# Performance work log

Measured on AMD Instinct MI355X. Metric: run time of the kernel, lower is better.

The kernel has to match this reference:

```python
import jax, jax.numpy as jnp
import numpy as np

N, D, K = 65536, 128, 2048  # n_cells, latent_dim, nmb_prototypes


def setup_inputs() -> dict:
    key = jax.random.key(0)
    k1, k2, k3, k4, k5 = jax.random.split(key, 5)
    x = jax.random.normal(k1, (N, D), dtype=jnp.float32)
    # nn.Linear default init scale ~ 1/sqrt(fan_in)
    W_proto = jax.random.normal(k2, (K, D), dtype=jnp.float32) * (1.0 / np.sqrt(D))
    recon_loss = jax.random.uniform(k3, (), dtype=jnp.float32)
    kl_loss = jax.random.uniform(k4, (), dtype=jnp.float32)
    mmd_loss = jax.random.uniform(k5, (), dtype=jnp.float32)
    return {"x": x, "W_proto": W_proto, "recon_loss": recon_loss,
            "kl_loss": kl_loss, "mmd_loss": mmd_loss}


def _pairwise_dist(z, w):
    # torch.cdist(z, w, p=2) via the matmul expansion (use_mm_for_euclid_dist)
    zz = jnp.sum(z * z, axis=1, keepdims=True)       # [N, 1]
    ww = jnp.sum(w * w, axis=1, keepdims=True).T     # [1, K]
    sq = zz + ww - 2.0 * (z @ w.T)                   # [N, K]
    return jnp.sqrt(jnp.maximum(sq, 0.0))


def reference(x, W_proto, recon_loss, kl_loss, mmd_loss):
    # cvae loss combination (compute_cvae_loss, calc_alpha_coeff = 0.5)
    cvae_loss = recon_loss + 0.5 * kl_loss + mmd_loss
    # F.normalize(x, dim=1, p=2): x / max(||x||_2, eps)
    nrm = jnp.maximum(jnp.linalg.norm(x, axis=1, keepdims=True), 1e-12)
    z = x / nrm                                      # [N, D]
    # self.prototypes(x): Linear without bias
    logits = z @ W_proto.T                           # [N, K]
    # prototype_decoding_loss: one NxK distance matrix reduced two ways
    dist = _pairwise_dist(z, W_proto)                # [N, K]
    propagation = jnp.mean(jnp.min(dist, axis=1))    # nearest prototype per cell
    emb_similarity = jnp.mean(jnp.min(dist, axis=0))  # nearest cell per prototype
    # forward returns (x, x, prototypes(x), cvae_loss, (prop, emb_sim)); x duplicated
    return (z, logits, cvae_loss, propagation, emb_similarity)
```

## Files before the change

### kernel.cpp

```cpp
#include <hip/hip_runtime.h>
#include <hip/hip_bf16.h>
#include <math.h>

#define N_CELLS 65536
#define D_DIM   128
#define K_PROTO 2048

typedef __attribute__((ext_vector_type(8))) short bf16x8;
typedef __attribute__((ext_vector_type(4))) float f32x4;

__device__ __forceinline__ unsigned int map_f2u(float f) {
  unsigned int u = __float_as_uint(f);
  return (u & 0x80000000u) ? ~u : (u | 0x80000000u);
}
__device__ __forceinline__ float unmap_u2f(unsigned int u) {
  unsigned int b = (u & 0x80000000u) ? (u ^ 0x80000000u) : ~u;
  return __uint_as_float(b);
}

__device__ __forceinline__ unsigned int f2bf(float f) {
  unsigned int u = __float_as_uint(f);
  return ((u + 0x7FFFu + ((u >> 16) & 1u)) >> 16) & 0xFFFFu;
}

__global__ __launch_bounds__(256) void normalize_k(
    const float* __restrict__ x, float* __restrict__ z,
    unsigned int* __restrict__ zb, unsigned int* __restrict__ rowmin_u) {
  int tid = threadIdx.x;
  int sub = tid & 31;
  int row = blockIdx.x * 8 + (tid >> 5);
  const f32x4* xr = (const f32x4*)(x + (size_t)row * D_DIM);
  f32x4 v = xr[sub];
  float s = v.x * v.x + v.y * v.y + v.z * v.z + v.w * v.w;
  #pragma unroll
  for (int off = 1; off < 32; off <<= 1) s += __shfl_xor(s, off, 64);
  float inv = 1.0f / fmaxf(sqrtf(s), 1e-12f);
  f32x4 zv = v * inv;
  __builtin_nontemporal_store(zv, (f32x4*)(z + (size_t)row * D_DIM) + sub);
  unsigned int lo = (f2bf(zv.y) << 16) | f2bf(zv.x);
  unsigned int h2 = (f2bf(zv.w) << 16) | f2bf(zv.z);
  unsigned long long pk = ((unsigned long long)h2 << 32) | lo;
  *((unsigned long long*)(zb + (size_t)row * (D_DIM / 2)) + sub) = pk;
  if (sub == 0) rowmin_u[row] = 0xFFFFFFFFu;
}

__global__ __launch_bounds__(256) void wprep_k(
    const float* __restrict__ W, unsigned int* __restrict__ wb,
    float* __restrict__ ww, unsigned int* __restrict__ colmax_u,
    const float* __restrict__ recon, const float* __restrict__ kl,
    const float* __restrict__ mmd, float* __restrict__ scal) {
  if (blockIdx.x == 0 && threadIdx.x == 0) {
    scal[0] = recon[0] + 0.5f * kl[0] + mmd[0];
  }
  int tid = threadIdx.x;
  int sub = tid & 31;
  int row = blockIdx.x * 8 + (tid >> 5);
  const f32x4* wr = (const f32x4*)(W + (size_t)row * D_DIM);
  f32x4 v = wr[sub];
  float s = v.x * v.x + v.y * v.y + v.z * v.z + v.w * v.w;
  #pragma unroll
  for (int off = 1; off < 32; off <<= 1) s += __shfl_xor(s, off, 64);
  if (sub == 0) {
    ww[row] = s;
    colmax_u[row] = 0u;
  }
  unsigned int lo = (f2bf(v.y) << 16) | f2bf(v.x);
  unsigned int h2 = (f2bf(v.w) << 16) | f2bf(v.z);
  unsigned long long pk = ((unsigned long long)h2 << 32) | lo;
  *((unsigned long long*)(wb + (size_t)row * (D_DIM / 2)) + sub) = pk;
}

__global__ __launch_bounds__(256) void gemm_k(
    const unsigned short* __restrict__ zb, const unsigned short* __restrict__ wb,
    const float* __restrict__ ww, float* __restrict__ logits,
    unsigned int* __restrict__ rowmin_u, unsigned int* __restrict__ colmax_u) {
  __shared__ float cs[128 * 128];

  int bid = blockIdx.x;
  int swz = (bid & 7) * 1024 + (bid >> 3);
  int nt  = swz & 15;
  int mt  = swz >> 4;

  int tid  = threadIdx.x;
  int lane = tid & 63;
  int wid  = tid >> 6;
  int wrow = (wid >> 1) * 64;
  int wcol = (wid & 1) * 64;
  int l15  = lane & 15;
  int hi   = lane >> 4;

  const char* Abase = (const char*)zb + ((size_t)(mt * 128 + wrow + l15) * 256 + hi * 16);
  const char* Bbase = (const char*)wb + ((size_t)(nt * 128 + wcol + l15) * 256 + hi * 16);

  f32x4 acc[4][4];
  #pragma unroll
  for (int i = 0; i < 4; ++i)
    #pragma unroll
    for (int j = 0; j < 4; ++j)
      acc[i][j] = f32x4{0.f, 0.f, 0.f, 0.f};

  #pragma unroll
  for (int kk = 0; kk < 4; ++kk) {
    bf16x8 a[4], b[4];
    #pragma unroll
    for (int i = 0; i < 4; ++i) a[i] = *(const bf16x8*)(Abase + i * 4096 + kk * 64);
    #pragma unroll
    for (int j = 0; j < 4; ++j) b[j] = *(const bf16x8*)(Bbase + j * 4096 + kk * 64);
    #pragma unroll
    for (int i = 0; i < 4; ++i)
      #pragma unroll
      for (int j = 0; j < 4; ++j)
        acc[i][j] = __builtin_amdgcn_mfma_f32_16x16x32_bf16(b[j], a[i], acc[i][j], 0, 0, 0);
  }

  size_t growbase = (size_t)mt * 128 + wrow;
  int    gcolbase = nt * 128 + wcol;

  f32x4 wwj[4];
  #pragma unroll
  for (int j = 0; j < 4; ++j)
    wwj[j] = *(const f32x4*)(ww + gcolbase + j * 16 + hi * 4);

  #pragma unroll
  for (int i = 0; i < 4; ++i) {
    size_t row = growbase + (size_t)(i * 16 + l15);
    float vmin = 1e30f;
    #pragma unroll
    for (int j = 0; j < 4; ++j) {
      #pragma unroll
      for (int r = 0; r < 4; ++r) vmin = fminf(vmin, wwj[j][r] - 2.0f * acc[i][j][r]);
    }
    vmin = fminf(vmin, __shfl_xor(vmin, 16, 64));
    vmin = fminf(vmin, __shfl_xor(vmin, 32, 64));
    if (hi == 0) atomicMin(&rowmin_u[row], map_f2u(vmin));
  }

  #pragma unroll
  for (int j = 0; j < 4; ++j) {
    f32x4 m = acc[0][j];
    #pragma unroll
    for (int i = 1; i < 4; ++i)
      #pragma unroll
      for (int r = 0; r < 4; ++r) m[r] = fmaxf(m[r], acc[i][j][r]);
    #pragma unroll
    for (int s2 = 1; s2 < 16; s2 <<= 1)
      #pragma unroll
      for (int r = 0; r < 4; ++r) m[r] = fmaxf(m[r], __shfl_xor(m[r], s2, 64));
    if (l15 == 0) {
      #pragma unroll
      for (int r = 0; r < 4; ++r)
        atomicMax(&colmax_u[gcolbase + j * 16 + hi * 4 + r], map_f2u(m[r]));
    }
  }

  #pragma unroll
  for (int i = 0; i < 4; ++i) {
    int row = wrow + i * 16 + l15;
    #pragma unroll
    for (int j = 0; j < 4; ++j) {
      int g  = (wcol >> 2) + j * 4 + hi;
      int pg = g ^ ((row & 7) << 2);
      *(f32x4*)((char*)cs + row * 512 + pg * 16) = acc[i][j];
    }
  }
  __syncthreads();

  {
    int l31  = lane & 31;
    int rsub = lane >> 5;
    #pragma unroll
    for (int it = 0; it < 16; ++it) {
      int row = it * 8 + wid * 2 + rsub;
      int pg  = l31 ^ ((row & 7) << 2);
      f32x4 c = *(const f32x4*)((const char*)cs + row * 512 + pg * 16);
      size_t grow = (size_t)mt * 128 + row;
      __builtin_nontemporal_store(c, (f32x4*)(logits + grow * K_PROTO + nt * 128 + l31 * 4));
    }
  }
}

__global__ __launch_bounds__(1024) void prop_k(
    const unsigned int* __restrict__ rowmin_u, float* __restrict__ out) {
  __shared__ float sbuf[16];
  const uint4* p = (const uint4*)rowmin_u;
  float s = 0.f;
  #pragma unroll
  for (int k = 0; k < 16; ++k) {
    uint4 u = p[threadIdx.x + 1024 * k];
    s += sqrtf(fmaxf(1.0f + unmap_u2f(u.x), 0.0f));
    s += sqrtf(fmaxf(1.0f + unmap_u2f(u.y), 0.0f));
    s += sqrtf(fmaxf(1.0f + unmap_u2f(u.z), 0.0f));
    s += sqrtf(fmaxf(1.0f + unmap_u2f(u.w), 0.0f));
  }
  #pragma unroll
  for (int off = 1; off < 64; off <<= 1) s += __shfl_xor(s, off, 64);
  int wid = threadIdx.x >> 6, lane = threadIdx.x & 63;
  if (lane == 0) sbuf[wid] = s;
  __syncthreads();
  if (threadIdx.x == 0) {
    float t = 0.f;
    #pragma unroll
    for (int w = 0; w < 16; ++w) t += sbuf[w];
    out[0] = t * (1.0f / N_CELLS);
  }
}

__global__ __launch_bounds__(1024) void emb_k(
    const unsigned int* __restrict__ colmax_u, const float* __restrict__ ww,
    float* __restrict__ out) {
  __shared__ float sbuf[16];
  float s = 0.f;
  for (int idx = threadIdx.x; idx < K_PROTO; idx += 1024)
    s += sqrtf(fmaxf(1.0f + ww[idx] - 2.0f * unmap_u2f(colmax_u[idx]), 0.0f));
  #pragma unroll
  for (int off = 1; off < 64; off <<= 1) s += __shfl_xor(s, off, 64);
  int wid = threadIdx.x >> 6, lane = threadIdx.x & 63;
  if (lane == 0) sbuf[wid] = s;
  __syncthreads();
  if (threadIdx.x == 0) {
    float t = 0.f;
    #pragma unroll
    for (int w = 0; w < 16; ++w) t += sbuf[w];
    out[0] = t * (1.0f / K_PROTO);
  }
}

extern "C" void kernel_launch(void* const* d_in, const int* in_sizes, int n_in,
                              void* d_out, int out_size, void* d_ws, size_t ws_size,
                              hipStream_t stream) {
  const float* x     = (const float*)d_in[0];
  const float* W     = (const float*)d_in[1];
  const float* recon = (const float*)d_in[2];
  const float* kl    = (const float*)d_in[3];
  const float* mmd   = (const float*)d_in[4];

  float* out    = (float*)d_out;
  float* z      = out;
  float* logits = out + (size_t)N_CELLS * D_DIM;
  float* scal   = logits + (size_t)N_CELLS * K_PROTO;

  char* ws = (char*)d_ws;
  unsigned int* zb = (unsigned int*)ws;
  size_t off = (size_t)N_CELLS * D_DIM * 2;
  unsigned int* wb = (unsigned int*)(ws + off);
  off += (size_t)K_PROTO * D_DIM * 2;
  float* ww = (float*)(ws + off);
  off += (size_t)K_PROTO * 4;
  unsigned int* rowmin_u = (unsigned int*)(ws + off);
  off += (size_t)N_CELLS * 4;
  unsigned int* colmax_u = (unsigned int*)(ws + off);

  normalize_k<<<N_CELLS / 8, 256, 0, stream>>>(x, z, zb, rowmin_u);
  wprep_k<<<K_PROTO / 8, 256, 0, stream>>>(W, wb, ww, colmax_u, recon, kl, mmd, scal);
  gemm_k<<<(N_CELLS / 128) * (K_PROTO / 128), 256, 0, stream>>>(
      (const unsigned short*)zb, (const unsigned short*)wb, ww, logits,
      rowmin_u, colmax_u);
  prop_k<<<1, 1024, 0, stream>>>(rowmin_u, scal + 1);
  emb_k<<<1, 1024, 0, stream>>>(colmax_u, ww, scal + 2);
}
```

Measured before the change: 206.4 us.

## Replace global atomic min/max with per-tile partials and multi-block reductions

The GEMM epilogue no longer issues global atomicMin/atomicMax for row minima and column maxima. Each tile now combines its warp results in shared memory and writes one partial per row and column to workspace buffers. Separate multi-block kernels reduce those partials, and a small final kernel combines the block sums. This removes atomic contention and the init writes, at the cost of an extra launch and more workspace traffic (about 4MB each for row and column partials).

```diff
diff --git a/kernel.cpp b/kernel.cpp
--- a/kernel.cpp
+++ b/kernel.cpp
@@ -9,15 +9,6 @@
 typedef __attribute__((ext_vector_type(8))) short bf16x8;
 typedef __attribute__((ext_vector_type(4))) float f32x4;
 
-__device__ __forceinline__ unsigned int map_f2u(float f) {
-  unsigned int u = __float_as_uint(f);
-  return (u & 0x80000000u) ? ~u : (u | 0x80000000u);
-}
-__device__ __forceinline__ float unmap_u2f(unsigned int u) {
-  unsigned int b = (u & 0x80000000u) ? (u ^ 0x80000000u) : ~u;
-  return __uint_as_float(b);
-}
-
 __device__ __forceinline__ unsigned int f2bf(float f) {
   unsigned int u = __float_as_uint(f);
   return ((u + 0x7FFFu + ((u >> 16) & 1u)) >> 16) & 0xFFFFu;
@@ -25,7 +16,7 @@
 
 __global__ __launch_bounds__(256) void normalize_k(
     const float* __restrict__ x, float* __restrict__ z,
-    unsigned int* __restrict__ zb, unsigned int* __restrict__ rowmin_u) {
+    unsigned int* __restrict__ zb) {
   int tid = threadIdx.x;
   int sub = tid & 31;
   int row = blockIdx.x * 8 + (tid >> 5);
@@ -41,12 +32,11 @@
   unsigned int h2 = (f2bf(zv.w) << 16) | f2bf(zv.z);
   unsigned long long pk = ((unsigned long long)h2 << 32) | lo;
   *((unsigned long long*)(zb + (size_t)row * (D_DIM / 2)) + sub) = pk;
-  if (sub == 0) rowmin_u[row] = 0xFFFFFFFFu;
 }
 
 __global__ __launch_bounds__(256) void wprep_k(
     const float* __restrict__ W, unsigned int* __restrict__ wb,
-    float* __restrict__ ww, unsigned int* __restrict__ colmax_u,
+    float* __restrict__ ww,
     const float* __restrict__ recon, const float* __restrict__ kl,
     const float* __restrict__ mmd, float* __restrict__ scal) {
   if (blockIdx.x == 0 && threadIdx.x == 0) {
@@ -60,10 +50,7 @@
   float s = v.x * v.x + v.y * v.y + v.z * v.z + v.w * v.w;
   #pragma unroll
   for (int off = 1; off < 32; off <<= 1) s += __shfl_xor(s, off, 64);
-  if (sub == 0) {
-    ww[row] = s;
-    colmax_u[row] = 0u;
-  }
+  if (sub == 0) ww[row] = s;
   unsigned int lo = (f2bf(v.y) << 16) | f2bf(v.x);
   unsigned int h2 = (f2bf(v.w) << 16) | f2bf(v.z);
   unsigned long long pk = ((unsigned long long)h2 << 32) | lo;
@@ -73,8 +60,10 @@
 __global__ __launch_bounds__(256) void gemm_k(
     const unsigned short* __restrict__ zb, const unsigned short* __restrict__ wb,
     const float* __restrict__ ww, float* __restrict__ logits,
-    unsigned int* __restrict__ rowmin_u, unsigned int* __restrict__ colmax_u) {
+    float* __restrict__ rowmin_part, float* __restrict__ colmax_part) {
   __shared__ float cs[128 * 128];
+  __shared__ float rmin[2][128];
+  __shared__ float cmx[2][128];
 
   int bid = blockIdx.x;
   int swz = (bid & 7) * 1024 + (bid >> 3);
@@ -113,9 +102,7 @@
         acc[i][j] = __builtin_amdgcn_mfma_f32_16x16x32_bf16(b[j], a[i], acc[i][j], 0, 0, 0);
   }
 
-  size_t growbase = (size_t)mt * 128 + wrow;
-  int    gcolbase = nt * 128 + wcol;
-
+  int gcolbase = nt * 128 + wcol;
   f32x4 wwj[4];
   #pragma unroll
   for (int j = 0; j < 4; ++j)
@@ -123,16 +110,14 @@
 
   #pragma unroll
   for (int i = 0; i < 4; ++i) {
-    size_t row = growbase + (size_t)(i * 16 + l15);
     float vmin = 1e30f;
     #pragma unroll
-    for (int j = 0; j < 4; ++j) {
+    for (int j = 0; j < 4; ++j)
       #pragma unroll
       for (int r = 0; r < 4; ++r) vmin = fminf(vmin, wwj[j][r] - 2.0f * acc[i][j][r]);
-    }
     vmin = fminf(vmin, __shfl_xor(vmin, 16, 64));
     vmin = fminf(vmin, __shfl_xor(vmin, 32, 64));
-    if (hi == 0) atomicMin(&rowmin_u[row], map_f2u(vmin));
+    if (hi == 0) rmin[wid & 1][wrow + i * 16 + l15] = vmin;
   }
 
   #pragma unroll
@@ -146,11 +131,8 @@
     for (int s2 = 1; s2 < 16; s2 <<= 1)
       #pragma unroll
       for (int r = 0; r < 4; ++r) m[r] = fmaxf(m[r], __shfl_xor(m[r], s2, 64));
-    if (l15 == 0) {
-      #pragma unroll
-      for (int r = 0; r < 4; ++r)
-        atomicMax(&colmax_u[gcolbase + j * 16 + hi * 4 + r], map_f2u(m[r]));
-    }
+    if (l15 == 0)
+      *(f32x4*)&cmx[wid >> 1][wcol + j * 16 + hi * 4] = m;
   }
 
   #pragma unroll
@@ -164,6 +146,15 @@
     }
   }
   __syncthreads();
+
+  if (tid < 128) {
+    rowmin_part[(size_t)nt * N_CELLS + mt * 128 + tid] =
+        fminf(rmin[0][tid], rmin[1][tid]);
+  } else {
+    int c = tid - 128;
+    colmax_part[(size_t)mt * K_PROTO + nt * 128 + c] =
+        fmaxf(cmx[0][c], cmx[1][c]);
+  }
 
   {
     int l31  = lane & 31;
@@ -179,49 +170,68 @@
   }
 }
 
-__global__ __launch_bounds__(1024) void prop_k(
-    const unsigned int* __restrict__ rowmin_u, float* __restrict__ out) {
+__global__ __launch_bounds__(1024) void prop1_k(
+    const float* __restrict__ rowmin_part, float* __restrict__ prop_part) {
   __shared__ float sbuf[16];
-  const uint4* p = (const uint4*)rowmin_u;
+  int slot = blockIdx.x * 1024 + threadIdx.x;
+  f32x4 v = *(const f32x4*)(rowmin_part + (size_t)slot * 4);
+  #pragma unroll
+  for (int p = 1; p < 16; ++p) {
+    f32x4 u = *(const f32x4*)(rowmin_part + (size_t)p * N_CELLS + (size_t)slot * 4);
+    #pragma unroll
+    for (int r = 0; r < 4; ++r) v[r] = fminf(v[r], u[r]);
+  }
   float s = 0.f;
   #pragma unroll
-  for (int k = 0; k < 16; ++k) {
-    uint4 u = p[threadIdx.x + 1024 * k];
-    s += sqrtf(fmaxf(1.0f + unmap_u2f(u.x), 0.0f));
-    s += sqrtf(fmaxf(1.0f + unmap_u2f(u.y), 0.0f));
-    s += sqrtf(fmaxf(1.0f + unmap_u2f(u.z), 0.0f));
-    s += sqrtf(fmaxf(1.0f + unmap_u2f(u.w), 0.0f));
-  }
+  for (int r = 0; r < 4; ++r) s += sqrtf(fmaxf(1.0f + v[r], 0.0f));
   #pragma unroll
   for (int off = 1; off < 64; off <<= 1) s += __shfl_xor(s, off, 64);
-  int wid = threadIdx.x >> 6, lane = threadIdx.x & 63;
-  if (lane == 0) sbuf[wid] = s;
+  int wv = threadIdx.x >> 6, lane = threadIdx.x & 63;
+  if (lane == 0) sbuf[wv] = s;
   __syncthreads();
   if (threadIdx.x == 0) {
     float t = 0.f;
     #pragma unroll
     for (int w = 0; w < 16; ++w) t += sbuf[w];
-    out[0] = t * (1.0f / N_CELLS);
-  }
-}
-
-__global__ __launch_bounds__(1024) void emb_k(
-    const unsigned int* __restrict__ colmax_u, const float* __restrict__ ww,
-    float* __restrict__ out) {
-  __shared__ float sbuf[16];
-  float s = 0.f;
-  for (int idx = threadIdx.x; idx < K_PROTO; idx += 1024)
-    s += sqrtf(fmaxf(1.0f + ww[idx] - 2.0f * unmap_u2f(colmax_u[idx]), 0.0f));
-  #pragma unroll
-  for (int off = 1; off < 64; off <<= 1) s += __shfl_xor(s, off, 64);
-  int wid = threadIdx.x >> 6, lane = threadIdx.x & 63;
-  if (lane == 0) sbuf[wid] = s;
-  __syncthreads();
+    prop_part[blockIdx.x] = t;
+  }
+}
+
+__global__ __launch_bounds__(1024) void emb1_k(
+    const float* __restrict__ colmax_part, const float* __restrict__ ww,
+    float* __restrict__ emb_part) {
+  __shared__ float buf[8][128];
+  __shared__ float sbuf[2];
+  int t   = threadIdx.x;
+  int col = blockIdx.x * 128 + (t & 127);
+  int seg = t >> 7;
+  float m = -1e30f;
+  for (int k = 0; k < 64; ++k)
+    m = fmaxf(m, colmax_part[(size_t)(seg * 64 + k) * K_PROTO + col]);
+  buf[seg][t & 127] = m;
+  __syncthreads();
+  if (t < 128) {
+    float tot = buf[0][t];
+    #pragma unroll
+    for (int s2 = 1; s2 < 8; ++s2) tot = fmaxf(tot, buf[s2][t]);
+    float val = sqrtf(fmaxf(1.0f + ww[col] - 2.0f * tot, 0.0f));
+    #pragma unroll
+    for (int off = 1; off < 64; off <<= 1) val += __shfl_xor(val, off, 64);
+    if ((t & 63) == 0) sbuf[t >> 6] = val;
+  }
+  __syncthreads();
+  if (t == 0) emb_part[blockIdx.x] = sbuf[0] + sbuf[1];
+}
+
+__global__ __launch_bounds__(64) void final_k(
+    const float* __restrict__ prop_part, const float* __restrict__ emb_part,
+    float* __restrict__ scal) {
   if (threadIdx.x == 0) {
-    float t = 0.f;
-    #pragma unroll
-    for (int w = 0; w < 16; ++w) t += sbuf[w];
-    out[0] = t * (1.0f / K_PROTO);
+    float p = 0.f, e = 0.f;
+    #pragma unroll
+    for (int i = 0; i < 16; ++i) { p += prop_part[i]; e += emb_part[i]; }
+    scal[1] = p * (1.0f / N_CELLS);
+    scal[2] = e * (1.0f / K_PROTO);
   }
 }
 
@@ -246,15 +256,20 @@
   off += (size_t)K_PROTO * D_DIM * 2;
   float* ww = (float*)(ws + off);
   off += (size_t)K_PROTO * 4;
-  unsigned int* rowmin_u = (unsigned int*)(ws + off);
-  off += (size_t)N_CELLS * 4;
-  unsigned int* colmax_u = (unsigned int*)(ws + off);
-
-  normalize_k<<<N_CELLS / 8, 256, 0, stream>>>(x, z, zb, rowmin_u);
-  wprep_k<<<K_PROTO / 8, 256, 0, stream>>>(W, wb, ww, colmax_u, recon, kl, mmd, scal);
+  float* rowmin_part = (float*)(ws + off);
+  off += (size_t)16 * N_CELLS * 4;
+  float* colmax_part = (float*)(ws + off);
+  off += (size_t)512 * K_PROTO * 4;
+  float* prop_part = (float*)(ws + off);
+  off += 16 * 4;
+  float* emb_part = (float*)(ws + off);
+
+  normalize_k<<<N_CELLS / 8, 256, 0, stream>>>(x, z, zb);
+  wprep_k<<<K_PROTO / 8, 256, 0, stream>>>(W, wb, ww, recon, kl, mmd, scal);
   gemm_k<<<(N_CELLS / 128) * (K_PROTO / 128), 256, 0, stream>>>(
       (const unsigned short*)zb, (const unsigned short*)wb, ww, logits,
-      rowmin_u, colmax_u);
-  prop_k<<<1, 1024, 0, stream>>>(rowmin_u, scal + 1);
-  emb_k<<<1, 1024, 0, stream>>>(colmax_u, ww, scal + 2);
-}
+      rowmin_part, colmax_part);
+  prop1_k<<<16, 1024, 0, stream>>>(rowmin_part, prop_part);
+  emb1_k<<<16, 1024, 0, stream>>>(colmax_part, ww, emb_part);
+  final_k<<<1, 64, 0, stream>>>(prop_part, emb_part, scal);
+}
```

Result: faster. 191.9 us (median of 2 runs) (-7.0%).
